# Kernel optimization log

Hardware: AMD Instinct MI355X
Metric: run time of the kernel (lower is better)

Reference implementation:

```python
import jax, jax.numpy as jnp
from jax import lax
import numpy as np

C = 64      # channels
K = 3       # dynamic kernel size
N = 2       # batch
H = 256
W = 256
DOWN = 4    # avgpool factor


def _conv(x, w, b):
    # 'SAME' padding matches get_same_padding for odd kernels, dilation=1
    y = lax.conv_general_dilated(x, w, (1, 1), 'SAME',
                                 dimension_numbers=('NCHW', 'OIHW', 'NCHW'))
    return y + b[None, :, None, None]


def _resblock(x, w1, b1, w2, b2):
    out = jax.nn.leaky_relu(_conv(x, w1, b1), 0.1)
    return _conv(out, w2, b2) + x


def _block(x, ws1, bs1, ws2, bs2):
    # fixed small loop over 3 structurally distinct ResBlocks
    for i in range(ws1.shape[0]):
        x = _resblock(x, ws1[i], bs1[i], ws2[i], bs2[i])
    return x


def _avgpool(x, k):
    n, c, h, w = x.shape
    return x.reshape(n, c, h // k, k, w // k, k).mean(axis=(3, 5))


def _maxpool(x, k):
    n, c, h, w = x.shape
    return x.reshape(n, c, h // k, k, w // k, k).max(axis=(3, 5))


def _dyn_conv(x, wt, k):
    # per-pixel depthwise conv: out[n,c,h,w] = sum_{dh,dw} xpad[n,c,h+dh,w+dw] * wt[n, c*k*k + dh*k + dw, h, w]
    # (torch's unfold/permute flattening pairs feat tap (dh,dw) with kernel channel index dh*k+dw)
    n, c, h, w = x.shape
    pad = (k - 1) // 2
    xp = jnp.pad(x, ((0, 0), (0, 0), (pad, pad), (pad, pad)), mode='edge')  # replicate pad
    wr = wt.reshape(n, c, k * k, h, w)
    out = jnp.zeros_like(x)
    for dh in range(k):            # fixed 3x3 tap loop; avoids materializing the unfold tensor
        for dw in range(k):
            out = out + xp[:, :, dh:dh + h, dw:dw + w] * wr[:, :, dh * k + dw]
    return out


def setup_inputs() -> dict:
    key = jax.random.key(0)
    ks = jax.random.split(key, 11)
    s = 0.05  # small init so 6 residual blocks stay numerically tame
    return {
        'x': jax.random.normal(ks[0], (N, C, H, W), jnp.float32),
        'blk1_w1': jax.random.normal(ks[1], (3, C, C, K, K), jnp.float32) * s,
        'blk1_b1': jnp.zeros((3, C), jnp.float32),
        'blk1_w2': jax.random.normal(ks[2], (3, C, C, K, K), jnp.float32) * s,
        'blk1_b2': jnp.zeros((3, C), jnp.float32),
        'blk2_w1': jax.random.normal(ks[3], (3, C, C, K, K), jnp.float32) * s,
        'blk2_b1': jnp.zeros((3, C), jnp.float32),
        'blk2_w2': jax.random.normal(ks[4], (3, C, C, K, K), jnp.float32) * s,
        'blk2_b2': jnp.zeros((3, C), jnp.float32),
        'tok_w': jax.random.normal(ks[5], (K * K * C, C, 1, 1), jnp.float32) * s,
        'tok_b': jnp.zeros((K * K * C,), jnp.float32),
    }


def reference(x, blk1_w1, blk1_b1, blk1_w2, blk1_b2,
              blk2_w1, blk2_b1, blk2_w2, blk2_b2, tok_w, tok_b):
    y = _avgpool(x, DOWN)                                   # [N,C,H/4,W/4]
    y = _block(y, blk1_w1, blk1_b1, blk1_w2, blk1_b2)
    y = _maxpool(y, 2)                                      # [N,C,H/8,W/8]
    y = _block(y, blk2_w1, blk2_b1, blk2_w2, blk2_b2)
    wt = _conv(y, tok_w, tok_b)                             # [N,9C,H/8,W/8]
    n, ck2, hs, ws = wt.shape
    # F.interpolate(scale_factor=2*down, mode='bilinear', align_corners=False)
    wt = jax.image.resize(wt, (n, ck2, hs * 2 * DOWN, ws * 2 * DOWN), method='bilinear')
    return _dyn_conv(x, wt, K)
```

## Files before the change

kernel.cpp:

```cpp
#include <hip/hip_runtime.h>


__global__ __launch_bounds__(256) void avgpool4_k(const float* __restrict__ x,
                                                  float* __restrict__ y) {
    int idx = blockIdx.x * 256 + threadIdx.x;
    int wo = idx & 63;
    int ho = (idx >> 6) & 63;
    int cz = idx >> 12;
    const float* base = x + ((long)cz * 256 + ho * 4) * 256 + wo * 4;
    float s = 0.f;
#pragma unroll
    for (int r = 0; r < 4; ++r) {
        float4 v = *(const float4*)(base + r * 256);
        s += v.x + v.y + v.z + v.w;
    }
    y[idx] = s * 0.0625f;
}

template <int S, int CIB>
__global__ __launch_bounds__(256, 2) void conv3x3s_k(
    const float* __restrict__ in, const float* __restrict__ wgt,
    float* __restrict__ outp) {
    constexpr int KSN = 64 / CIB;
    constexpr int T = 16;
    constexpr int NT1 = S / T;
    constexpr int NT = NT1 * NT1;
    constexpr int HW = T + 2;
    constexpr int SROW = 20;
    constexpr int TOT = CIB * 18 * HW;
    constexpr int NLD = (TOT + 255) / 256;
    constexpr int TAIL = TOT - (NLD - 1) * 256;
    __shared__ __align__(16) float s_in[CIB * 18 * SROW];

    const int tid = threadIdx.x;
    int z = blockIdx.x;
    const int ks = z % KSN; z /= KSN;
    const int ocg = z & 3; z >>= 2;
    const int tile = z % NT;
    const int n = z / NT;
    const int th0 = (tile / NT1) * T, tw0 = (tile % NT1) * T;
    const int oc0 = ocg * 16;

    const float* inb = in + ((long)n * 64 + ks * CIB) * (S * S);
#pragma unroll
    for (int j = 0; j < NLD; ++j) {
        int idx = tid + j * 256;
        bool slot = (j < NLD - 1) || (tid < TAIL);
        int t = slot ? idx : 0;
        int ci = t / (18 * HW);
        int rem = t - ci * (18 * HW);
        int r = rem / HW;
        int c = rem - r * HW;
        int gh = th0 + r - 1, gw = tw0 + c - 1;
        float v = 0.f;
        if (slot && (unsigned)gh < (unsigned)S && (unsigned)gw < (unsigned)S)
            v = inb[ci * (S * S) + gh * S + gw];
        if (slot) s_in[ci * (18 * SROW) + r * SROW + c] = v;
    }
    __syncthreads();

    const int lane = tid & 63;
    const int wid = __builtin_amdgcn_readfirstlane(tid >> 6);
    const int lx = lane & 3;
    const int ly = lane >> 2;
    const int px0 = lx * 4;

    const float* wb = wgt + (long)(oc0 + wid * 4) * 576 + ks * (CIB * 9);

    float acc[4][4];
#pragma unroll
    for (int k = 0; k < 4; ++k)
#pragma unroll
        for (int p = 0; p < 4; ++p) acc[k][p] = 0.f;

#pragma unroll
    for (int ci = 0; ci < CIB; ++ci) {
        float xr[3][6];
#pragma unroll
        for (int r = 0; r < 3; ++r) {
            const float* rp = &s_in[ci * (18 * SROW) + (ly + r) * SROW + px0];
            float4 a = *(const float4*)rp;
            float2 b = *(const float2*)(rp + 4);
            xr[r][0] = a.x; xr[r][1] = a.y; xr[r][2] = a.z;
            xr[r][3] = a.w; xr[r][4] = b.x; xr[r][5] = b.y;
        }
#pragma unroll
        for (int k = 0; k < 4; ++k) {
            const float* wk = wb + k * 576 + ci * 9;
#pragma unroll
            for (int dh = 0; dh < 3; ++dh) {
                float w0 = wk[dh * 3 + 0];
                float w1 = wk[dh * 3 + 1];
                float w2 = wk[dh * 3 + 2];
#pragma unroll
                for (int p = 0; p < 4; ++p)
                    acc[k][p] += xr[dh][p] * w0 + xr[dh][p + 1] * w1 +
                                 xr[dh][p + 2] * w2;
            }
        }
    }

    const int gy = th0 + ly, gx = tw0 + px0;
    const long pstride = (long)2 * 64 * S * S;
    long off0 = ks * pstride +
                ((long)(n * 64 + oc0 + wid * 4)) * (S * S) + gy * S + gx;
#pragma unroll
    for (int k = 0; k < 4; ++k) {
        float4 v;
        v.x = acc[k][0]; v.y = acc[k][1]; v.z = acc[k][2]; v.w = acc[k][3];
        *(float4*)&outp[off0 + (long)k * (S * S)] = v;
    }
}

template <int NP, int SSLOG, bool LRELU, bool RES>
__global__ __launch_bounds__(256) void comb_k(
    const float* __restrict__ P, const float* __restrict__ bias,
    const float* __restrict__ res, float* __restrict__ out) {
    const long pstride = (long)2 * 64 << SSLOG;
    long base = ((long)blockIdx.x * 256 + threadIdx.x) * 4;
    int c = (int)((base >> SSLOG) & 63);
    float4 v = *(const float4*)&P[base];
#pragma unroll
    for (int p = 1; p < NP; ++p) {
        float4 u = *(const float4*)&P[base + p * pstride];
        v.x += u.x; v.y += u.y; v.z += u.z; v.w += u.w;
    }
    float b = bias[c];
    v.x += b; v.y += b; v.z += b; v.w += b;
    if (LRELU) {
        v.x = v.x > 0.f ? v.x : 0.1f * v.x;
        v.y = v.y > 0.f ? v.y : 0.1f * v.y;
        v.z = v.z > 0.f ? v.z : 0.1f * v.z;
        v.w = v.w > 0.f ? v.w : 0.1f * v.w;
    }
    if (RES) {
        float4 r = *(const float4*)&res[base];
        v.x += r.x; v.y += r.y; v.z += r.z; v.w += r.w;
    }
    *(float4*)&out[base] = v;
}

template <int NP>
__global__ __launch_bounds__(256) void maxpool_comb_k(
    const float* __restrict__ Pb, const float* __restrict__ bias,
    const float* __restrict__ res, float* __restrict__ P) {
    int idx = blockIdx.x * 256 + threadIdx.x;
    int wo = idx & 31;
    int ho = (idx >> 5) & 31;
    int cz = idx >> 10;
    float bch = bias[cz & 63];
    float m = -3.4e38f;
#pragma unroll
    for (int dh = 0; dh < 2; ++dh)
#pragma unroll
        for (int dw = 0; dw < 2; ++dw) {
            long off = ((long)cz * 64 + ho * 2 + dh) * 64 + wo * 2 + dw;
            float y = bch + res[off];
#pragma unroll
            for (int p = 0; p < NP; ++p) y += Pb[off + (long)p * 524288];
            m = fmaxf(m, y);
        }
    P[idx] = m;
}

__global__ __launch_bounds__(256) void conv1x1_k(
    const float* __restrict__ in, const float* __restrict__ w,
    const float* __restrict__ b, float* __restrict__ out) {
    __shared__ float s_in[32 * 256];
    __shared__ __align__(16) float s_w[64 * 8];
    const int tid = threadIdx.x;
    const int p0 = blockIdx.x * 256;
    const int cog = blockIdx.y;
    const int n = blockIdx.z;

    for (int idx = tid; idx < 512; idx += 256) {
        int j = idx >> 6;
        int ci = idx & 63;
        s_w[ci * 8 + j] = w[(long)cog * 512 + idx];
    }

    float acc[8];
#pragma unroll
    for (int i = 0; i < 8; ++i) acc[i] = b[cog * 8 + i];

    float pf[32];
#pragma unroll
    for (int i = 0; i < 32; ++i)
        pf[i] = in[(long)(n * 64 + i) * 1024 + p0 + tid];

    for (int chunk = 0; chunk < 64; chunk += 32) {
        __syncthreads();
#pragma unroll
        for (int i = 0; i < 32; ++i) s_in[i * 256 + tid] = pf[i];
        __syncthreads();
        if (chunk + 32 < 64) {
#pragma unroll
            for (int i = 0; i < 32; ++i)
                pf[i] = in[(long)(n * 64 + chunk + 32 + i) * 1024 + p0 + tid];
        }
#pragma unroll 4
        for (int ci = 0; ci < 32; ++ci) {
            float v = s_in[ci * 256 + tid];
            float4 w0 = *(const float4*)&s_w[(chunk + ci) * 8];
            float4 w1 = *(const float4*)&s_w[(chunk + ci) * 8 + 4];
            acc[0] += v * w0.x; acc[1] += v * w0.y;
            acc[2] += v * w0.z; acc[3] += v * w0.w;
            acc[4] += v * w1.x; acc[5] += v * w1.y;
            acc[6] += v * w1.z; acc[7] += v * w1.w;
        }
    }
#pragma unroll
    for (int oc = 0; oc < 8; ++oc)
        out[(long)(n * 576 + cog * 8 + oc) * 1024 + p0 + tid] = acc[oc];
}

__global__ __launch_bounds__(256) void dynconv_k(
    const float* __restrict__ x, const float* __restrict__ wt,
    float* __restrict__ out) {
    __shared__ __align__(16) float s_x[10 * 132];
    __shared__ float s_wt[9 * 60];
    const int tid = threadIdx.x;
    const int tx = tid & 31;
    const int ty = tid >> 5;
    const int tw = (blockIdx.x & 1) * 128;
    const int th = (blockIdx.x >> 1) * 8;
    const int cz = blockIdx.y;

    const float* xb = x + (long)cz * 65536;
    for (int idx = tid; idx < 1300; idx += 256) {
        int r = idx / 130;
        int c = idx - r * 130;
        int gh = min(max(th + r - 1, 0), 255);
        int gw = min(max(tw + c - 1, 0), 255);
        s_x[r * 132 + c] = xb[gh * 256 + gw];
    }

    const int h0min = th / 8 - 1;
    const int w0min = tw / 8 - 1;
    const float* wtb = wt + (long)cz * 9 * 1024;
    for (int i = tid; i < 540; i += 256) {
        int tap = i / 60;
        int rem = i - tap * 60;
        int r = rem / 20;
        int c = rem - r * 20;
        if (c < 18) {
            int gr = min(max(h0min + r, 0), 31);
            int gc = min(max(w0min + c, 0), 31);
            s_wt[i] = wtb[tap * 1024 + gr * 32 + gc];
        }
    }

    const int h = th + ty;
    const int wbase = tw + tx * 4;
    float src_h = h * 0.125f - 0.4375f;
    int h0 = (int)floorf(src_h);
    float fh = src_h - (float)h0;
    int r0 = h0 - h0min;
    float src_w = wbase * 0.125f - 0.4375f;
    int w0 = (int)floorf(src_w);
    float fw0 = src_w - (float)w0;
    int j = w0 - w0min;

    __syncthreads();

    float vals[3][6];
#pragma unroll
    for (int r = 0; r < 3; ++r) {
        const float* rp = &s_x[(ty + r) * 132 + tx * 4];
        float4 a = *(const float4*)rp;
        float2 b = *(const float2*)(rp + 4);
        vals[r][0] = a.x; vals[r][1] = a.y; vals[r][2] = a.z;
        vals[r][3] = a.w; vals[r][4] = b.x; vals[r][5] = b.y;
    }

    float acc[4] = {0.f, 0.f, 0.f, 0.f};
#pragma unroll
    for (int dh = 0; dh < 3; ++dh)
#pragma unroll
        for (int dw = 0; dw < 3; ++dw) {
            const float* p = &s_wt[(dh * 3 + dw) * 60 + r0 * 20 + j];
            float t0 = p[0], t1 = p[1];
            float b0 = p[20], b1 = p[21];
            float c0 = t0 + fh * (b0 - t0);
            float c1 = t1 + fh * (b1 - t1);
            float d = c1 - c0;
#pragma unroll
            for (int jj = 0; jj < 4; ++jj) {
                float wv = c0 + (fw0 + 0.125f * jj) * d;
                acc[jj] += vals[dh][jj + dw] * wv;
            }
        }

    float4 o;
    o.x = acc[0]; o.y = acc[1]; o.z = acc[2]; o.w = acc[3];
    *(float4*)&out[(long)cz * 65536 + h * 256 + wbase] = o;
}

extern "C" void kernel_launch(void* const* d_in, const int* in_sizes, int n_in,
                              void* d_out, int out_size, void* d_ws, size_t ws_size,
                              hipStream_t stream) {
    const float* x    = (const float*)d_in[0];
    const float* b1w1 = (const float*)d_in[1];
    const float* b1b1 = (const float*)d_in[2];
    const float* b1w2 = (const float*)d_in[3];
    const float* b1b2 = (const float*)d_in[4];
    const float* b2w1 = (const float*)d_in[5];
    const float* b2b1 = (const float*)d_in[6];
    const float* b2w2 = (const float*)d_in[7];
    const float* b2b2 = (const float*)d_in[8];
    const float* tokw = (const float*)d_in[9];
    const float* tokb = (const float*)d_in[10];
    float* out = (float*)d_out;
    float* ws = (float*)d_ws;

    float* X0 = ws;
    float* X1 = ws + 524288;
    float* T  = ws + 1048576;
    float* P  = ws + 1572864;
    float* Pm = ws + 5767168;
    float* Q  = ws + 5898240;
    float* U  = ws + 6029312;
    float* WT = ws + 6160384;

    const int WSZ = 64 * 64 * 9;

    avgpool4_k<<<2048, 256, 0, stream>>>(x, X0);

    conv3x3s_k<64, 16><<<512, 256, 0, stream>>>(X0, b1w1 + 0 * WSZ, P);
    comb_k<4, 12, true,  false><<<512, 256, 0, stream>>>(P, b1b1 + 0, nullptr, T);
    conv3x3s_k<64, 16><<<512, 256, 0, stream>>>(T, b1w2 + 0 * WSZ, P);
    comb_k<4, 12, false, true ><<<512, 256, 0, stream>>>(P, b1b2 + 0, X0, X1);

    conv3x3s_k<64, 16><<<512, 256, 0, stream>>>(X1, b1w1 + 1 * WSZ, P);
    comb_k<4, 12, true,  false><<<512, 256, 0, stream>>>(P, b1b1 + 64, nullptr, T);
    conv3x3s_k<64, 16><<<512, 256, 0, stream>>>(T, b1w2 + 1 * WSZ, P);
    comb_k<4, 12, false, true ><<<512, 256, 0, stream>>>(P, b1b2 + 64, X1, X0);

    conv3x3s_k<64, 16><<<512, 256, 0, stream>>>(X0, b1w1 + 2 * WSZ, P);
    comb_k<4, 12, true,  false><<<512, 256, 0, stream>>>(P, b1b1 + 128, nullptr, T);
    conv3x3s_k<64, 16><<<512, 256, 0, stream>>>(T, b1w2 + 2 * WSZ, P);
    maxpool_comb_k<4><<<512, 256, 0, stream>>>(P, b1b2 + 128, X0, Pm);

    conv3x3s_k<32, 8><<<256, 256, 0, stream>>>(Pm, b2w1 + 0 * WSZ, P);
    comb_k<8, 10, true,  false><<<128, 256, 0, stream>>>(P, b2b1 + 0, nullptr, U);
    conv3x3s_k<32, 8><<<256, 256, 0, stream>>>(U, b2w2 + 0 * WSZ, P);
    comb_k<8, 10, false, true ><<<128, 256, 0, stream>>>(P, b2b2 + 0, Pm, Q);

    conv3x3s_k<32, 8><<<256, 256, 0, stream>>>(Q, b2w1 + 1 * WSZ, P);
    comb_k<8, 10, true,  false><<<128, 256, 0, stream>>>(P, b2b1 + 64, nullptr, U);
    conv3x3s_k<32, 8><<<256, 256, 0, stream>>>(U, b2w2 + 1 * WSZ, P);
    comb_k<8, 10, false, true ><<<128, 256, 0, stream>>>(P, b2b2 + 64, Q, Pm);

    conv3x3s_k<32, 8><<<256, 256, 0, stream>>>(Pm, b2w1 + 2 * WSZ, P);
    comb_k<8, 10, true,  false><<<128, 256, 0, stream>>>(P, b2b1 + 128, nullptr, U);
    conv3x3s_k<32, 8><<<256, 256, 0, stream>>>(U, b2w2 + 2 * WSZ, P);
    comb_k<8, 10, false, true ><<<128, 256, 0, stream>>>(P, b2b2 + 128, Pm, Q);

    conv1x1_k<<<dim3(4, 72, 2), 256, 0, stream>>>(Q, tokw, tokb, WT);

    dynconv_k<<<dim3(64, 128), 256, 0, stream>>>(x, WT, out);
}
```

Baseline: 372.1 us.

## Fuse 3x3 conv split-K reduction with bias, activation, residual and maxpool epilogue

Replaces the split-K 3x3 conv plus separate combine kernels with one conv kernel per layer. It uses 512-thread blocks that split the input channels between two half-groups, reduces their partial sums through shared memory, and applies bias, leaky-ReLU, residual add or 2x2 maxpool in the epilogue. This removes the partial-sum buffer writes and reads and halves the number of launches. In exchange the grids are smaller (256 and 64 blocks) and each thread produces fewer outputs, which may lower GPU utilisation on the small 32x32 stage.

```diff
diff --git a/kernel.cpp b/kernel.cpp
--- a/kernel.cpp
+++ b/kernel.cpp
@@ -17,150 +17,134 @@
     y[idx] = s * 0.0625f;
 }
 
-template <int S, int CIB>
-__global__ __launch_bounds__(256, 2) void conv3x3s_k(
+template <int S, int VAR>
+__global__ __launch_bounds__(512) void conv3x3f_k(
     const float* __restrict__ in, const float* __restrict__ wgt,
+    const float* __restrict__ bias, const float* __restrict__ res,
     float* __restrict__ outp) {
-    constexpr int KSN = 64 / CIB;
-    constexpr int T = 16;
-    constexpr int NT1 = S / T;
-    constexpr int NT = NT1 * NT1;
-    constexpr int HW = T + 2;
+    constexpr int TH = 8, TW = 16;
+    constexpr int NTW = S / TW, NTH = S / TH;
+    constexpr int NT = NTW * NTH;
     constexpr int SROW = 20;
-    constexpr int TOT = CIB * 18 * HW;
-    constexpr int NLD = (TOT + 255) / 256;
-    constexpr int TAIL = TOT - (NLD - 1) * 256;
-    __shared__ __align__(16) float s_in[CIB * 18 * SROW];
+    constexpr int CHW = 10 * SROW;
+    constexpr int TOTS = 16 * 10 * 18;
+    constexpr int NLD = (TOTS + 511) / 512;
+    constexpr int TAIL = TOTS - (NLD - 1) * 512;
+    __shared__ __align__(16) float s_in[16 * CHW];
 
     const int tid = threadIdx.x;
     int z = blockIdx.x;
-    const int ks = z % KSN; z /= KSN;
     const int ocg = z & 3; z >>= 2;
     const int tile = z % NT;
     const int n = z / NT;
-    const int th0 = (tile / NT1) * T, tw0 = (tile % NT1) * T;
+    const int th0 = (tile / NTW) * TH, tw0 = (tile % NTW) * TW;
     const int oc0 = ocg * 16;
 
-    const float* inb = in + ((long)n * 64 + ks * CIB) * (S * S);
-#pragma unroll
-    for (int j = 0; j < NLD; ++j) {
-        int idx = tid + j * 256;
-        bool slot = (j < NLD - 1) || (tid < TAIL);
-        int t = slot ? idx : 0;
-        int ci = t / (18 * HW);
-        int rem = t - ci * (18 * HW);
-        int r = rem / HW;
-        int c = rem - r * HW;
-        int gh = th0 + r - 1, gw = tw0 + c - 1;
-        float v = 0.f;
-        if (slot && (unsigned)gh < (unsigned)S && (unsigned)gw < (unsigned)S)
-            v = inb[ci * (S * S) + gh * S + gw];
-        if (slot) s_in[ci * (18 * SROW) + r * SROW + c] = v;
-    }
+    const int lane = tid & 63;
+    const int wid8 = __builtin_amdgcn_readfirstlane(tid >> 6);
+    const int widq = wid8 & 3;
+    const int half = wid8 >> 2;
+    const int lx = lane & 7;
+    const int ly = lane >> 3;
+    const int px0 = lx * 2;
+
+    const float* inb = in + (long)n * 64 * (S * S);
+    const float* wb = wgt + (long)(oc0 + widq * 4) * 576 + (half * 32) * 9;
+
+    float acc[4][2];
+#pragma unroll
+    for (int k = 0; k < 4; ++k) { acc[k][0] = 0.f; acc[k][1] = 0.f; }
+
+    for (int step = 0; step < 4; ++step) {
+        __syncthreads();
+#pragma unroll
+        for (int j = 0; j < NLD; ++j) {
+            int idx = tid + j * 512;
+            bool slot = (j < NLD - 1) || (tid < TAIL);
+            int t = slot ? idx : 0;
+            int ch = t / 180;
+            int rem = t - ch * 180;
+            int r = rem / 18;
+            int c = rem - r * 18;
+            int gci = (ch >> 3) * 32 + step * 8 + (ch & 7);
+            int gh = th0 + r - 1, gw = tw0 + c - 1;
+            float v = 0.f;
+            if (slot && (unsigned)gh < (unsigned)S && (unsigned)gw < (unsigned)S)
+                v = inb[(long)gci * (S * S) + gh * S + gw];
+            if (slot) s_in[ch * CHW + r * SROW + c] = v;
+        }
+        __syncthreads();
+#pragma unroll
+        for (int cc = 0; cc < 8; ++cc) {
+            float xr[3][4];
+#pragma unroll
+            for (int r = 0; r < 3; ++r) {
+                const float* rp =
+                    &s_in[(half * 8 + cc) * CHW + (ly + r) * SROW + px0];
+                float2 a = *(const float2*)rp;
+                float2 b = *(const float2*)(rp + 2);
+                xr[r][0] = a.x; xr[r][1] = a.y; xr[r][2] = b.x; xr[r][3] = b.y;
+            }
+            const float* wk0 = wb + (step * 8 + cc) * 9;
+#pragma unroll
+            for (int k = 0; k < 4; ++k) {
+                const float* wk = wk0 + k * 576;
+#pragma unroll
+                for (int dh = 0; dh < 3; ++dh) {
+                    float w0 = wk[dh * 3 + 0];
+                    float w1 = wk[dh * 3 + 1];
+                    float w2 = wk[dh * 3 + 2];
+                    acc[k][0] += xr[dh][0] * w0 + xr[dh][1] * w1 + xr[dh][2] * w2;
+                    acc[k][1] += xr[dh][1] * w0 + xr[dh][2] * w1 + xr[dh][3] * w2;
+                }
+            }
+        }
+    }
+
     __syncthreads();
-
-    const int lane = tid & 63;
-    const int wid = __builtin_amdgcn_readfirstlane(tid >> 6);
-    const int lx = lane & 3;
-    const int ly = lane >> 2;
-    const int px0 = lx * 4;
-
-    const float* wb = wgt + (long)(oc0 + wid * 4) * 576 + ks * (CIB * 9);
-
-    float acc[4][4];
-#pragma unroll
-    for (int k = 0; k < 4; ++k)
-#pragma unroll
-        for (int p = 0; p < 4; ++p) acc[k][p] = 0.f;
-
-#pragma unroll
-    for (int ci = 0; ci < CIB; ++ci) {
-        float xr[3][6];
-#pragma unroll
-        for (int r = 0; r < 3; ++r) {
-            const float* rp = &s_in[ci * (18 * SROW) + (ly + r) * SROW + px0];
-            float4 a = *(const float4*)rp;
-            float2 b = *(const float2*)(rp + 4);
-            xr[r][0] = a.x; xr[r][1] = a.y; xr[r][2] = a.z;
-            xr[r][3] = a.w; xr[r][4] = b.x; xr[r][5] = b.y;
-        }
+    if (half == 1) {
 #pragma unroll
         for (int k = 0; k < 4; ++k) {
-            const float* wk = wb + k * 576 + ci * 9;
-#pragma unroll
-            for (int dh = 0; dh < 3; ++dh) {
-                float w0 = wk[dh * 3 + 0];
-                float w1 = wk[dh * 3 + 1];
-                float w2 = wk[dh * 3 + 2];
-#pragma unroll
-                for (int p = 0; p < 4; ++p)
-                    acc[k][p] += xr[dh][p] * w0 + xr[dh][p + 1] * w1 +
-                                 xr[dh][p + 2] * w2;
+            s_in[(k * 2 + 0) * 256 + widq * 64 + lane] = acc[k][0];
+            s_in[(k * 2 + 1) * 256 + widq * 64 + lane] = acc[k][1];
+        }
+    }
+    __syncthreads();
+    if (half == 0) {
+        const int gy = th0 + ly, gx = tw0 + px0;
+#pragma unroll
+        for (int k = 0; k < 4; ++k) {
+            float y0 = acc[k][0] + s_in[(k * 2 + 0) * 256 + widq * 64 + lane];
+            float y1 = acc[k][1] + s_in[(k * 2 + 1) * 256 + widq * 64 + lane];
+            float bv = bias[oc0 + widq * 4 + k];
+            y0 += bv; y1 += bv;
+            long po = ((long)(n * 64 + oc0 + widq * 4 + k)) * (S * S) +
+                      gy * S + gx;
+            if (VAR == 0) {
+                y0 = y0 > 0.f ? y0 : 0.1f * y0;
+                y1 = y1 > 0.f ? y1 : 0.1f * y1;
+                float2 o; o.x = y0; o.y = y1;
+                *(float2*)&outp[po] = o;
+            } else if (VAR == 1) {
+                float2 rv = *(const float2*)&res[po];
+                float2 o; o.x = y0 + rv.x; o.y = y1 + rv.y;
+                *(float2*)&outp[po] = o;
+            } else {
+                float2 rv = *(const float2*)&res[po];
+                y0 += rv.x; y1 += rv.y;
+                float m = fmaxf(y0, y1);
+                float o = __shfl_xor(m, 8);
+                m = fmaxf(m, o);
+                if ((ly & 1) == 0) {
+                    constexpr int SP = S / 2;
+                    long qo = ((long)(n * 64 + oc0 + widq * 4 + k)) *
+                                  (SP * SP) +
+                              (gy >> 1) * SP + (tw0 >> 1) + lx;
+                    outp[qo] = m;
+                }
             }
         }
     }
-
-    const int gy = th0 + ly, gx = tw0 + px0;
-    const long pstride = (long)2 * 64 * S * S;
-    long off0 = ks * pstride +
-                ((long)(n * 64 + oc0 + wid * 4)) * (S * S) + gy * S + gx;
-#pragma unroll
-    for (int k = 0; k < 4; ++k) {
-        float4 v;
-        v.x = acc[k][0]; v.y = acc[k][1]; v.z = acc[k][2]; v.w = acc[k][3];
-        *(float4*)&outp[off0 + (long)k * (S * S)] = v;
-    }
-}
-
-template <int NP, int SSLOG, bool LRELU, bool RES>
-__global__ __launch_bounds__(256) void comb_k(
-    const float* __restrict__ P, const float* __restrict__ bias,
-    const float* __restrict__ res, float* __restrict__ out) {
-    const long pstride = (long)2 * 64 << SSLOG;
-    long base = ((long)blockIdx.x * 256 + threadIdx.x) * 4;
-    int c = (int)((base >> SSLOG) & 63);
-    float4 v = *(const float4*)&P[base];
-#pragma unroll
-    for (int p = 1; p < NP; ++p) {
-        float4 u = *(const float4*)&P[base + p * pstride];
-        v.x += u.x; v.y += u.y; v.z += u.z; v.w += u.w;
-    }
-    float b = bias[c];
-    v.x += b; v.y += b; v.z += b; v.w += b;
-    if (LRELU) {
-        v.x = v.x > 0.f ? v.x : 0.1f * v.x;
-        v.y = v.y > 0.f ? v.y : 0.1f * v.y;
-        v.z = v.z > 0.f ? v.z : 0.1f * v.z;
-        v.w = v.w > 0.f ? v.w : 0.1f * v.w;
-    }
-    if (RES) {
-        float4 r = *(const float4*)&res[base];
-        v.x += r.x; v.y += r.y; v.z += r.z; v.w += r.w;
-    }
-    *(float4*)&out[base] = v;
-}
-
-template <int NP>
-__global__ __launch_bounds__(256) void maxpool_comb_k(
-    const float* __restrict__ Pb, const float* __restrict__ bias,
-    const float* __restrict__ res, float* __restrict__ P) {
-    int idx = blockIdx.x * 256 + threadIdx.x;
-    int wo = idx & 31;
-    int ho = (idx >> 5) & 31;
-    int cz = idx >> 10;
-    float bch = bias[cz & 63];
-    float m = -3.4e38f;
-#pragma unroll
-    for (int dh = 0; dh < 2; ++dh)
-#pragma unroll
-        for (int dw = 0; dw < 2; ++dw) {
-            long off = ((long)cz * 64 + ho * 2 + dh) * 64 + wo * 2 + dw;
-            float y = bch + res[off];
-#pragma unroll
-            for (int p = 0; p < NP; ++p) y += Pb[off + (long)p * 524288];
-            m = fmaxf(m, y);
-        }
-    P[idx] = m;
 }
 
 __global__ __launch_bounds__(256) void conv1x1_k(
@@ -316,45 +300,28 @@
     float* X0 = ws;
     float* X1 = ws + 524288;
     float* T  = ws + 1048576;
-    float* P  = ws + 1572864;
-    float* Pm = ws + 5767168;
-    float* Q  = ws + 5898240;
-    float* U  = ws + 6029312;
-    float* WT = ws + 6160384;
+    float* Pm = ws + 1572864;
+    float* Q  = ws + 1703936;
+    float* U  = ws + 1835008;
+    float* WT = ws + 1966080;
 
     const int WSZ = 64 * 64 * 9;
 
     avgpool4_k<<<2048, 256, 0, stream>>>(x, X0);
 
-    conv3x3s_k<64, 16><<<512, 256, 0, stream>>>(X0, b1w1 + 0 * WSZ, P);
-    comb_k<4, 12, true,  false><<<512, 256, 0, stream>>>(P, b1b1 + 0, nullptr, T);
-    conv3x3s_k<64, 16><<<512, 256, 0, stream>>>(T, b1w2 + 0 * WSZ, P);
-    comb_k<4, 12, false, true ><<<512, 256, 0, stream>>>(P, b1b2 + 0, X0, X1);
-
-    conv3x3s_k<64, 16><<<512, 256, 0, stream>>>(X1, b1w1 + 1 * WSZ, P);
-    comb_k<4, 12, true,  false><<<512, 256, 0, stream>>>(P, b1b1 + 64, nullptr, T);
-    conv3x3s_k<64, 16><<<512, 256, 0, stream>>>(T, b1w2 + 1 * WSZ, P);
-    comb_k<4, 12, false, true ><<<512, 256, 0, stream>>>(P, b1b2 + 64, X1, X0);
-
-    conv3x3s_k<64, 16><<<512, 256, 0, stream>>>(X0, b1w1 + 2 * WSZ, P);
-    comb_k<4, 12, true,  false><<<512, 256, 0, stream>>>(P, b1b1 + 128, nullptr, T);
-    conv3x3s_k<64, 16><<<512, 256, 0, stream>>>(T, b1w2 + 2 * WSZ, P);
-    maxpool_comb_k<4><<<512, 256, 0, stream>>>(P, b1b2 + 128, X0, Pm);
-
-    conv3x3s_k<32, 8><<<256, 256, 0, stream>>>(Pm, b2w1 + 0 * WSZ, P);
-    comb_k<8, 10, true,  false><<<128, 256, 0, stream>>>(P, b2b1 + 0, nullptr, U);
-    conv3x3s_k<32, 8><<<256, 256, 0, stream>>>(U, b2w2 + 0 * WSZ, P);
-    comb_k<8, 10, false, true ><<<128, 256, 0, stream>>>(P, b2b2 + 0, Pm, Q);
-
-    conv3x3s_k<32, 8><<<256, 256, 0, stream>>>(Q, b2w1 + 1 * WSZ, P);
-    comb_k<8, 10, true,  false><<<128, 256, 0, stream>>>(P, b2b1 + 64, nullptr, U);
-    conv3x3s_k<32, 8><<<256, 256, 0, stream>>>(U, b2w2 + 1 * WSZ, P);
-    comb_k<8, 10, false, true ><<<128, 256, 0, stream>>>(P, b2b2 + 64, Q, Pm);
-
-    conv3x3s_k<32, 8><<<256, 256, 0, stream>>>(Pm, b2w1 + 2 * WSZ, P);
-    comb_k<8, 10, true,  false><<<128, 256, 0, stream>>>(P, b2b1 + 128, nullptr, U);
-    conv3x3s_k<32, 8><<<256, 256, 0, stream>>>(U, b2w2 + 2 * WSZ, P);
-    comb_k<8, 10, false, true ><<<128, 256, 0, stream>>>(P, b2b2 + 128, Pm, Q);
+    conv3x3f_k<64, 0><<<256, 512, 0, stream>>>(X0, b1w1 + 0 * WSZ, b1b1 + 0,   nullptr, T);
+    conv3x3f_k<64, 1><<<256, 512, 0, stream>>>(T,  b1w2 + 0 * WSZ, b1b2 + 0,   X0, X1);
+    conv3x3f_k<64, 0><<<256, 512, 0, stream>>>(X1, b1w1 + 1 * WSZ, b1b1 + 64,  nullptr, T);
+    conv3x3f_k<64, 1><<<256, 512, 0, stream>>>(T,  b1w2 + 1 * WSZ, b1b2 + 64,  X1, X0);
+    conv3x3f_k<64, 0><<<256, 512, 0, stream>>>(X0, b1w1 + 2 * WSZ, b1b1 + 128, nullptr, T);
+    conv3x3f_k<64, 2><<<256, 512, 0, stream>>>(T,  b1w2 + 2 * WSZ, b1b2 + 128, X0, Pm);
+
+    conv3x3f_k<32, 0><<<64, 512, 0, stream>>>(Pm, b2w1 + 0 * WSZ, b2b1 + 0,   nullptr, U);
+    conv3x3f_k<32, 1><<<64, 512, 0, stream>>>(U,  b2w2 + 0 * WSZ, b2b2 + 0,   Pm, Q);
+    conv3x3f_k<32, 0><<<64, 512, 0, stream>>>(Q,  b2w1 + 1 * WSZ, b2b1 + 64,  nullptr, U);
+    conv3x3f_k<32, 1><<<64, 512, 0, stream>>>(U,  b2w2 + 1 * WSZ, b2b2 + 64,  Q, Pm);
+    conv3x3f_k<32, 0><<<64, 512, 0, stream>>>(Pm, b2w1 + 2 * WSZ, b2b1 + 128, nullptr, U);
+    conv3x3f_k<32, 1><<<64, 512, 0, stream>>>(U,  b2w2 + 2 * WSZ, b2b2 + 128, Pm, Q);
 
     conv1x1_k<<<dim3(4, 72, 2), 256, 0, stream>>>(Q, tokw, tokb, WT);
 
```

Result: slower. 449.0 us (+20.7%).
